# Kernel tuning notes

Hardware: AMD Instinct MI355X
Metric: run time of the kernel (lower is better)

## Reference

```python
import jax, jax.numpy as jnp
import numpy as np

# Performer/FAVOR+ style linear attention constants (from module __init__)
A_CONST = 0.1
S_CONST = 1.0
B_CONST = (S_CONST * (1.0 - 4.0 * A_CONST)) ** 0.5  # sqrt(0.6)
C_CONST = -(S_CONST + 1.0) / 2.0                    # -1.0

R = 256     # number of random features
D = 64      # head / feature dim
L = 65536   # sequence length
DV = 64     # value dim
SCALE = 0.125  # keep ||q||^2 ~ 1 so exp stays well-conditioned


def setup_inputs() -> dict:
    key = jax.random.key(0)
    kq, kk, kv, kw = jax.random.split(key, 4)
    Q = jax.random.normal(kq, (D, L), dtype=jnp.float32) * SCALE
    K = jax.random.normal(kk, (D, L), dtype=jnp.float32) * SCALE
    V = jax.random.normal(kv, (L, DV), dtype=jnp.float32)
    W = jax.random.normal(kw, (R, D), dtype=jnp.float32)  # random feature projections
    return {"Q": Q, "K": K, "V": V, "W": W}


def _phi(W, X, c):
    # X: [d, L]; W: [r, d] -> features [r, L]
    d = X.shape[0]
    D_norm = (1.0 - 4.0 * A_CONST) ** (d / 4.0)  # pow(pow(1-4A,0.25), d)
    sq = jnp.sum(X * X, axis=0)                  # [L], diag of X^T X
    return D_norm * jnp.exp(A_CONST + B_CONST * (W @ X) + c * sq)


def reference(Q, K, V, W):
    phiK = _phi(W, K, C_CONST * S_CONST)  # f2: [r, Lk]
    kv = phiK @ V                          # [r, dv]
    phiQ = _phi(W, Q, C_CONST)             # f1: [r, Lq]
    return phiQ.T @ kv                     # [Lq, dv]
```

## Files before the change

kernel.cpp:

```cpp
#include <hip/hip_runtime.h>

typedef _Float16 f16;
typedef __attribute__((ext_vector_type(8))) _Float16 f16x8;
typedef __attribute__((ext_vector_type(4))) _Float16 f16x4;
typedef __attribute__((ext_vector_type(4))) float f32x4;

#define BARRIER()                                              \
    do {                                                       \
        asm volatile("s_waitcnt lgkmcnt(0)" ::: "memory");     \
        __builtin_amdgcn_s_barrier();                          \
        __builtin_amdgcn_sched_barrier(0);                     \
    } while (0)

namespace {
constexpr int kL   = 65536;
constexpr int kR   = 256;
constexpr int kD   = 64;
constexpr int kDV  = 64;

constexpr int kChunks  = 4;
constexpr int kABlocks = 256;
constexpr int kBBlocks = 256;
constexpr int kRBlocks = 128;

constexpr float kBc   = 0.7745966692414834f;
constexpr float kBase0 = -1.1417405264f;
constexpr float kOutScale = 9.5367431640625e-7f;
}

__global__ __launch_bounds__(512, 2)
void favor_kv(const float* __restrict__ Kg, const float* __restrict__ Vg,
              const float* __restrict__ Wg, f16* __restrict__ partials)
{
    __shared__ f16 sXt[2][64 * 64];
    __shared__ f16 sVt[3][64 * 64];
    __shared__ f16 sPhi[2][256 * 64];
    __shared__ float sRed[2][8 * 64];
    __shared__ float sRedT[2][64];

    const int tid  = threadIdx.x;
    const int w    = tid >> 6;
    const int lane = tid & 63;
    const int l15  = lane & 15;
    const int lhi  = lane >> 4;
    const int blk  = blockIdx.x;
    const int lblk = blk * (64 * kChunks);

    const int scol  = lane;
    const int dbase = w * 8;
    const int wr = w >> 1;
    const int wc = w & 1;

    float ka[2][8], va[2][8];
    auto issueLoads = [&](int c) {
        const int l0 = lblk + c * 64;
        const int p  = c & 1;
#pragma unroll
        for (int j = 0; j < 8; ++j) ka[p][j] = Kg[(dbase + j) * kL + l0 + scol];
#pragma unroll
        for (int j = 0; j < 8; ++j) va[p][j] = Vg[(size_t)(l0 + dbase + j) * kDV + scol];
    };

    issueLoads(0);
    issueLoads(1);

    f16x8 wfrag[2][2];
#pragma unroll
    for (int ri = 0; ri < 2; ++ri)
#pragma unroll
        for (int ks = 0; ks < 2; ++ks) {
            const float* p = Wg + (32 * w + 16 * ri + l15) * kD + 32 * ks + 8 * lhi;
            f16x8 v;
#pragma unroll
            for (int j = 0; j < 8; ++j) v[j] = (f16)p[j];
            wfrag[ri][ks] = v;
        }

    f32x4 acc[4][2];
#pragma unroll
    for (int a = 0; a < 4; ++a)
#pragma unroll
        for (int d = 0; d < 2; ++d) { f32x4 z0 = {0.f, 0.f, 0.f, 0.f}; acc[a][d] = z0; }

    auto stage = [&](int c) {
        const int p  = c & 1;
        const int pv3 = c % 3;
        float s = 0.f;
        f16x8 hk, hv;
#pragma unroll
        for (int j = 0; j < 8; ++j) {
            const float x = ka[p][j];
            s += x * x;
            hk[j] = (f16)x;
            hv[j] = (f16)va[p][j];
        }
        sRed[p][w * 64 + scol] = s;
        *(f16x8*)&sXt[p][scol * 64 + (dbase ^ ((scol & 7) << 3))] = hk;
        *(f16x8*)&sVt[pv3][scol * 64 + (dbase ^ ((scol & 7) << 3))] = hv;
    };

    auto norms = [&](int c) {
        const int p = c & 1;
        float sqv = 0.f;
#pragma unroll
        for (int g = 0; g < 8; ++g) sqv += sRed[p][g * 64 + lane];
        sRedT[p][lane] = sqv;
    };

    auto zphi = [&](int c) {
        const int p = c & 1;
        f16x8 bfr[2][4];
#pragma unroll
        for (int ks = 0; ks < 2; ++ks)
#pragma unroll
            for (int lf = 0; lf < 4; ++lf) {
                const int row = 16 * lf + l15;
                bfr[ks][lf] = *(const f16x8*)&sXt[p][row * 64 + ((32 * ks + 8 * lhi) ^ ((row & 7) << 3))];
            }
#pragma unroll
        for (int ri = 0; ri < 2; ++ri) {
            f32x4 z[4];
#pragma unroll
            for (int lf = 0; lf < 4; ++lf) { f32x4 z0 = {0.f, 0.f, 0.f, 0.f}; z[lf] = z0; }
            __builtin_amdgcn_s_setprio(1);
#pragma unroll
            for (int ks = 0; ks < 2; ++ks)
#pragma unroll
                for (int lf = 0; lf < 4; ++lf)
                    z[lf] = __builtin_amdgcn_mfma_f32_16x16x32_f16(bfr[ks][lf], wfrag[ri][ks], z[lf], 0, 0, 0);
            __builtin_amdgcn_s_setprio(0);
            const int r = 32 * w + 16 * ri + l15;
#pragma unroll
            for (int lf = 0; lf < 4; ++lf) {
                const f32x4 sq4 = *(const f32x4*)&sRedT[p][16 * lf + 4 * lhi];
                f16x4 ph;
#pragma unroll
                for (int j = 0; j < 4; ++j)
                    ph[j] = (f16)__expf(fmaf(z[lf][j], kBc, kBase0 - sq4[j]));
                const int lbase = 16 * lf + 4 * lhi;
                *(f16x4*)&sPhi[p][r * 64 + (lbase ^ ((r & 7) << 3))] = ph;
            }
        }
    };

    auto pv = [&](int c) {
        const int p  = c & 1;
        const int pv3 = c % 3;
        __builtin_amdgcn_s_setprio(1);
#pragma unroll
        for (int ks = 0; ks < 2; ++ks) {
            f16x8 af[4], bf[2];
#pragma unroll
            for (int ai = 0; ai < 4; ++ai) {
                const int r = 64 * wr + 16 * ai + l15;
                af[ai] = *(const f16x8*)&sPhi[p][r * 64 + ((32 * ks + 8 * lhi) ^ ((r & 7) << 3))];
            }
#pragma unroll
            for (int di = 0; di < 2; ++di) {
                const int dv = 32 * wc + 16 * di + l15;
                bf[di] = *(const f16x8*)&sVt[pv3][dv * 64 + ((32 * ks + 8 * lhi) ^ ((dv & 7) << 3))];
            }
#pragma unroll
            for (int ai = 0; ai < 4; ++ai)
#pragma unroll
                for (int di = 0; di < 2; ++di)
                    acc[ai][di] = __builtin_amdgcn_mfma_f32_16x16x32_f16(af[ai], bf[di], acc[ai][di], 0, 0, 0);
        }
        __builtin_amdgcn_s_setprio(0);
    };

    stage(0);
    BARRIER();
#pragma unroll
    for (int c = 0; c < kChunks; ++c) {
        if (c > 0) pv(c - 1);
        norms(c);
        zphi(c);
        if (c + 1 < kChunks) stage(c + 1);
        if (c + 2 < kChunks) issueLoads(c + 2);
        BARRIER();
    }
    pv(kChunks - 1);

    f16* po = partials + (size_t)blk * (kR * kDV);
#pragma unroll
    for (int ai = 0; ai < 4; ++ai)
#pragma unroll
        for (int di = 0; di < 2; ++di) {
            const int dv = 32 * wc + 16 * di + l15;
            f16x4 pk;
#pragma unroll
            for (int j = 0; j < 4; ++j) pk[j] = (f16)acc[ai][di][j];
            *(f16x4*)&po[dv * kR + 64 * wr + 16 * ai + 4 * lhi] = pk;
        }
}

__global__ __launch_bounds__(512)
void favor_reduce(const f16* __restrict__ partials, f16* __restrict__ kvT,
                  const float* __restrict__ Wg, f16* __restrict__ Wp)
{
    __shared__ float sAcc[32][128];
    const int tid  = threadIdx.x;
    const int slot = tid & 15;
    const int g    = tid >> 4;

    if (blockIdx.x == 0) {
#pragma unroll
        for (int it = 0; it < 4; ++it) {
            const int idx    = tid + it * 512;
            const int fragid = idx >> 6;
            const int ln     = idx & 63;
            const int rf = fragid >> 1, ks = fragid & 1;
            const float* src = Wg + (16 * rf + (ln & 15)) * kD + 32 * ks + 8 * (ln >> 4);
            f16x8 v;
#pragma unroll
            for (int j = 0; j < 8; ++j) v[j] = (f16)src[j];
            *(f16x8*)&Wp[(size_t)idx * 8] = v;
        }
    }

    const size_t obase = (size_t)blockIdx.x * 128 + slot * 8;
    float a[8] = {0.f, 0.f, 0.f, 0.f, 0.f, 0.f, 0.f, 0.f};
#pragma unroll 4
    for (int i = 0; i < 8; ++i) {
        const int s = g * 8 + i;
        const f16x8 v = *(const f16x8*)&partials[(size_t)s * (kR * kDV) + obase];
#pragma unroll
        for (int j = 0; j < 8; ++j) a[j] += (float)v[j];
    }
#pragma unroll
    for (int j = 0; j < 8; ++j) sAcc[g][slot * 8 + j] = a[j];
    __syncthreads();

    if (tid < 128) {
        float tot = 0.f;
#pragma unroll
        for (int gg = 0; gg < 32; ++gg) tot += sAcc[gg][tid];
        kvT[(size_t)blockIdx.x * 128 + tid] = (f16)tot;
    }
}

__global__ __launch_bounds__(512, 2)
void favor_out(const float* __restrict__ Qg, const f16* __restrict__ Wp,
               const f16* __restrict__ kvT, float* __restrict__ outg)
{
    __shared__ f16 sXt[2][64 * 64];
    __shared__ f16 sPhiT[2][64 * 256];
    __shared__ float sRed[2][8 * 64];

    const int tid  = threadIdx.x;
    const int w    = tid >> 6;
    const int lane = tid & 63;
    const int l15  = lane & 15;
    const int lhi  = lane >> 4;
    const int blk  = blockIdx.x;
    const int lblk = blk * (64 * kChunks);

    const int scol  = lane;
    const int dbase = w * 8;
    const int lfo = w >> 1;
    const int dvh = w & 1;

    float qa[2][8];
    auto issueLoads = [&](int c) {
        const int l0 = lblk + c * 64;
        const int p  = c & 1;
#pragma unroll
        for (int j = 0; j < 8; ++j) qa[p][j] = Qg[(dbase + j) * kL + l0 + scol];
    };

    issueLoads(0);
    issueLoads(1);

    f16x8 kvf[2][8];
#pragma unroll
    for (int di = 0; di < 2; ++di) {
        const int dv = 32 * dvh + 16 * di + l15;
#pragma unroll
        for (int ks = 0; ks < 8; ++ks)
            kvf[di][ks] = *(const f16x8*)&kvT[dv * kR + 32 * ks + 8 * lhi];
    }

    f16x8 wfrag[2][2];
#pragma unroll
    for (int ri = 0; ri < 2; ++ri)
#pragma unroll
        for (int ks = 0; ks < 2; ++ks)
            wfrag[ri][ks] = *(const f16x8*)&Wp[(size_t)((((2 * w + ri) * 2 + ks) * 64) + lane) * 8];

    auto stageQ = [&](int c) {
        const int p = c & 1;
        float s = 0.f;
        f16x8 hq;
#pragma unroll
        for (int j = 0; j < 8; ++j) {
            const float x = qa[p][j];
            s += x * x;
            hq[j] = (f16)x;
        }
        sRed[p][w * 64 + scol] = s;
        *(f16x8*)&sXt[p][scol * 64 + (dbase ^ ((scol & 7) << 3))] = hq;
    };

    auto zphiQ = [&](int c) {
        const int p = c & 1;
        float sqv = 0.f;
#pragma unroll
        for (int g = 0; g < 8; ++g) sqv += sRed[p][g * 64 + lane];
        float tbase[4];
#pragma unroll
        for (int lf = 0; lf < 4; ++lf)
            tbase[lf] = kBase0 - __shfl(sqv, lf * 16 + l15, 64);

        f16x8 bfr[2][4];
#pragma unroll
        for (int ks = 0; ks < 2; ++ks)
#pragma unroll
            for (int lf = 0; lf < 4; ++lf) {
                const int row = 16 * lf + l15;
                bfr[ks][lf] = *(const f16x8*)&sXt[p][row * 64 + ((32 * ks + 8 * lhi) ^ ((row & 7) << 3))];
            }
#pragma unroll
        for (int ri = 0; ri < 2; ++ri) {
            f32x4 z[4];
#pragma unroll
            for (int lf = 0; lf < 4; ++lf) { f32x4 z0 = {0.f, 0.f, 0.f, 0.f}; z[lf] = z0; }
            __builtin_amdgcn_s_setprio(1);
#pragma unroll
            for (int ks = 0; ks < 2; ++ks)
#pragma unroll
                for (int lf = 0; lf < 4; ++lf)
                    z[lf] = __builtin_amdgcn_mfma_f32_16x16x32_f16(wfrag[ri][ks], bfr[ks][lf], z[lf], 0, 0, 0);
            __builtin_amdgcn_s_setprio(0);
            const int r0 = 32 * w + 16 * ri + 4 * lhi;
#pragma unroll
            for (int lf = 0; lf < 4; ++lf) {
                const int lc = 16 * lf + l15;
                f16x4 ph;
#pragma unroll
                for (int j = 0; j < 4; ++j)
                    ph[j] = (f16)__expf(fmaf(z[lf][j], kBc, tbase[lf]));
                *(f16x4*)&sPhiT[p][lc * 256 + (r0 ^ ((lc & 7) << 3))] = ph;
            }
        }
    };

    auto pvOut = [&](int c) {
        const int p = c & 1;
        f32x4 oA[2], oB[2];
        { f32x4 z0 = {0.f, 0.f, 0.f, 0.f}; oA[0] = z0; oA[1] = z0; oB[0] = z0; oB[1] = z0; }
        const int lrow = 16 * lfo + l15;
        __builtin_amdgcn_s_setprio(1);
#pragma unroll
        for (int ks = 0; ks < 4; ++ks) {
            const f16x8 afA = *(const f16x8*)&sPhiT[p][lrow * 256 + ((32 * ks + 8 * lhi) ^ ((lrow & 7) << 3))];
            const f16x8 afB = *(const f16x8*)&sPhiT[p][lrow * 256 + ((32 * (ks + 4) + 8 * lhi) ^ ((lrow & 7) << 3))];
#pragma unroll
            for (int di = 0; di < 2; ++di) {
                oA[di] = __builtin_amdgcn_mfma_f32_16x16x32_f16(afA, kvf[di][ks], oA[di], 0, 0, 0);
                oB[di] = __builtin_amdgcn_mfma_f32_16x16x32_f16(afB, kvf[di][ks + 4], oB[di], 0, 0, 0);
            }
        }
        __builtin_amdgcn_s_setprio(0);
        const int l0 = lblk + c * 64;
#pragma unroll
        for (int di = 0; di < 2; ++di) {
            const f32x4 o2 = oA[di] + oB[di];
#pragma unroll
            for (int j = 0; j < 4; ++j) {
                const int ll = 16 * lfo + 4 * lhi + j;
                const int dv = 32 * dvh + 16 * di + l15;
                outg[(size_t)(l0 + ll) * kDV + dv] = o2[j] * kOutScale;
            }
        }
    };

    stageQ(0);
    BARRIER();
#pragma unroll
    for (int c = 0; c < kChunks; ++c) {
        if (c > 0) pvOut(c - 1);
        zphiQ(c);
        if (c + 1 < kChunks) stageQ(c + 1);
        if (c + 2 < kChunks) issueLoads(c + 2);
        BARRIER();
    }
    pvOut(kChunks - 1);
}

extern "C" void kernel_launch(void* const* d_in, const int* in_sizes, int n_in,
                              void* d_out, int out_size, void* d_ws, size_t ws_size,
                              hipStream_t stream)
{
    const float* Q = (const float*)d_in[0];
    const float* K = (const float*)d_in[1];
    const float* V = (const float*)d_in[2];
    const float* W = (const float*)d_in[3];
    float* out = (float*)d_out;

    f16* partials = (f16*)d_ws;
    f16* kvT = (f16*)((char*)d_ws + (size_t)kABlocks * kR * kDV * sizeof(f16));
    f16* Wp  = kvT + (size_t)kR * kDV;

    favor_kv<<<kABlocks, 512, 0, stream>>>(K, V, W, partials);
    favor_reduce<<<kRBlocks, 512, 0, stream>>>(partials, kvT, W, Wp);
    favor_out<<<kBBlocks, 512, 0, stream>>>(Q, Wp, kvT, out);

    (void)in_sizes; (void)n_in; (void)out_size; (void)ws_size;
}
```

Measured before the change: 35.92 us.

## Load Q directly into MFMA B-fragments, dropping LDS staging and reduction

After: 36.56 us. No clear change (+1.8%).

```diff
diff --git a/kernel.cpp b/kernel.cpp
--- a/kernel.cpp
+++ b/kernel.cpp
@@ -244,9 +244,7 @@
 void favor_out(const float* __restrict__ Qg, const f16* __restrict__ Wp,
                const f16* __restrict__ kvT, float* __restrict__ outg)
 {
-    __shared__ f16 sXt[2][64 * 64];
     __shared__ f16 sPhiT[2][64 * 256];
-    __shared__ float sRed[2][8 * 64];
 
     const int tid  = threadIdx.x;
     const int w    = tid >> 6;
@@ -256,21 +254,43 @@
     const int blk  = blockIdx.x;
     const int lblk = blk * (64 * kChunks);
 
-    const int scol  = lane;
-    const int dbase = w * 8;
+    const int lfq   = w & 3;
+    const int rhalf = w >> 2;
     const int lfo = w >> 1;
     const int dvh = w & 1;
 
-    float qa[2][8];
-    auto issueLoads = [&](int c) {
-        const int l0 = lblk + c * 64;
-        const int p  = c & 1;
-#pragma unroll
-        for (int j = 0; j < 8; ++j) qa[p][j] = Qg[(dbase + j) * kL + l0 + scol];
-    };
-
-    issueLoads(0);
-    issueLoads(1);
+    float vq[16];
+    auto issueQ = [&](int c) {
+        const int l0 = lblk + c * 64 + 16 * lfq + l15;
+#pragma unroll
+        for (int ks = 0; ks < 2; ++ks)
+#pragma unroll
+            for (int j = 0; j < 8; ++j)
+                vq[ks * 8 + j] = Qg[(32 * ks + 8 * lhi + j) * kL + l0];
+    };
+
+    f16x8 qfrag[2][2];
+    float tb[2];
+    auto cvtQ = [&](int c) {
+        const int p = c & 1;
+        float s = 0.f;
+#pragma unroll
+        for (int ks = 0; ks < 2; ++ks) {
+            f16x8 h;
+#pragma unroll
+            for (int j = 0; j < 8; ++j) {
+                const float x = vq[ks * 8 + j];
+                s += x * x;
+                h[j] = (f16)x;
+            }
+            qfrag[p][ks] = h;
+        }
+        s += __shfl_xor(s, 16);
+        s += __shfl_xor(s, 32);
+        tb[p] = kBase0 - s;
+    };
+
+    issueQ(0);
 
     f16x8 kvf[2][8];
 #pragma unroll
@@ -281,68 +301,35 @@
             kvf[di][ks] = *(const f16x8*)&kvT[dv * kR + 32 * ks + 8 * lhi];
     }
 
-    f16x8 wfrag[2][2];
-#pragma unroll
-    for (int ri = 0; ri < 2; ++ri)
-#pragma unroll
-        for (int ks = 0; ks < 2; ++ks)
-            wfrag[ri][ks] = *(const f16x8*)&Wp[(size_t)((((2 * w + ri) * 2 + ks) * 64) + lane) * 8];
-
-    auto stageQ = [&](int c) {
-        const int p = c & 1;
-        float s = 0.f;
-        f16x8 hq;
-#pragma unroll
-        for (int j = 0; j < 8; ++j) {
-            const float x = qa[p][j];
-            s += x * x;
-            hq[j] = (f16)x;
-        }
-        sRed[p][w * 64 + scol] = s;
-        *(f16x8*)&sXt[p][scol * 64 + (dbase ^ ((scol & 7) << 3))] = hq;
-    };
+    f16x8 wfrag[8][2];
+#pragma unroll
+    for (int f = 0; f < 8; ++f)
+#pragma unroll
+        for (int ks = 0; ks < 2; ++ks) {
+            const int rf = rhalf * 8 + f;
+            wfrag[f][ks] = *(const f16x8*)&Wp[(size_t)(((rf * 2 + ks) * 64) + lane) * 8];
+        }
+
+    cvtQ(0);
 
     auto zphiQ = [&](int c) {
         const int p = c & 1;
-        float sqv = 0.f;
-#pragma unroll
-        for (int g = 0; g < 8; ++g) sqv += sRed[p][g * 64 + lane];
-        float tbase[4];
-#pragma unroll
-        for (int lf = 0; lf < 4; ++lf)
-            tbase[lf] = kBase0 - __shfl(sqv, lf * 16 + l15, 64);
-
-        f16x8 bfr[2][4];
-#pragma unroll
-        for (int ks = 0; ks < 2; ++ks)
-#pragma unroll
-            for (int lf = 0; lf < 4; ++lf) {
-                const int row = 16 * lf + l15;
-                bfr[ks][lf] = *(const f16x8*)&sXt[p][row * 64 + ((32 * ks + 8 * lhi) ^ ((row & 7) << 3))];
-            }
-#pragma unroll
-        for (int ri = 0; ri < 2; ++ri) {
-            f32x4 z[4];
-#pragma unroll
-            for (int lf = 0; lf < 4; ++lf) { f32x4 z0 = {0.f, 0.f, 0.f, 0.f}; z[lf] = z0; }
-            __builtin_amdgcn_s_setprio(1);
-#pragma unroll
-            for (int ks = 0; ks < 2; ++ks)
-#pragma unroll
-                for (int lf = 0; lf < 4; ++lf)
-                    z[lf] = __builtin_amdgcn_mfma_f32_16x16x32_f16(wfrag[ri][ks], bfr[ks][lf], z[lf], 0, 0, 0);
-            __builtin_amdgcn_s_setprio(0);
-            const int r0 = 32 * w + 16 * ri + 4 * lhi;
-#pragma unroll
-            for (int lf = 0; lf < 4; ++lf) {
-                const int lc = 16 * lf + l15;
-                f16x4 ph;
-#pragma unroll
-                for (int j = 0; j < 4; ++j)
-                    ph[j] = (f16)__expf(fmaf(z[lf][j], kBc, tbase[lf]));
-                *(f16x4*)&sPhiT[p][lc * 256 + (r0 ^ ((lc & 7) << 3))] = ph;
-            }
-        }
+        const int lc = 16 * lfq + l15;
+        const int m  = (lc & 7) << 3;
+        __builtin_amdgcn_s_setprio(1);
+#pragma unroll
+        for (int f = 0; f < 8; ++f) {
+            f32x4 z = {0.f, 0.f, 0.f, 0.f};
+            z = __builtin_amdgcn_mfma_f32_16x16x32_f16(wfrag[f][0], qfrag[p][0], z, 0, 0, 0);
+            z = __builtin_amdgcn_mfma_f32_16x16x32_f16(wfrag[f][1], qfrag[p][1], z, 0, 0, 0);
+            const int r0 = rhalf * 128 + f * 16 + 4 * lhi;
+            f16x4 ph;
+#pragma unroll
+            for (int j = 0; j < 4; ++j)
+                ph[j] = (f16)__expf(fmaf(z[j], kBc, tb[p]));
+            *(f16x4*)&sPhiT[p][lc * 256 + (r0 ^ m)] = ph;
+        }
+        __builtin_amdgcn_s_setprio(0);
     };
 
     auto pvOut = [&](int c) {
@@ -350,11 +337,12 @@
         f32x4 oA[2], oB[2];
         { f32x4 z0 = {0.f, 0.f, 0.f, 0.f}; oA[0] = z0; oA[1] = z0; oB[0] = z0; oB[1] = z0; }
         const int lrow = 16 * lfo + l15;
+        const int m = (lrow & 7) << 3;
         __builtin_amdgcn_s_setprio(1);
 #pragma unroll
         for (int ks = 0; ks < 4; ++ks) {
-            const f16x8 afA = *(const f16x8*)&sPhiT[p][lrow * 256 + ((32 * ks + 8 * lhi) ^ ((lrow & 7) << 3))];
-            const f16x8 afB = *(const f16x8*)&sPhiT[p][lrow * 256 + ((32 * (ks + 4) + 8 * lhi) ^ ((lrow & 7) << 3))];
+            const f16x8 afA = *(const f16x8*)&sPhiT[p][lrow * 256 + ((32 * ks + 8 * lhi) ^ m)];
+            const f16x8 afB = *(const f16x8*)&sPhiT[p][lrow * 256 + ((32 * (ks + 4) + 8 * lhi) ^ m)];
 #pragma unroll
             for (int di = 0; di < 2; ++di) {
                 oA[di] = __builtin_amdgcn_mfma_f32_16x16x32_f16(afA, kvf[di][ks], oA[di], 0, 0, 0);
@@ -375,15 +363,13 @@
         }
     };
 
-    stageQ(0);
-    BARRIER();
 #pragma unroll
     for (int c = 0; c < kChunks; ++c) {
         if (c > 0) pvOut(c - 1);
         zphiQ(c);
-        if (c + 1 < kChunks) stageQ(c + 1);
-        if (c + 2 < kChunks) issueLoads(c + 2);
+        if (c + 1 < kChunks) issueQ(c + 1);
         BARRIER();
+        if (c + 1 < kChunks) cvtQ(c + 1);
     }
     pvOut(kChunks - 1);
 }
```

## Replace partials buffer and reduce kernel with float atomics into kv accumulator

Applied to the files above, without the earlier changes.

New measurement: 137.1 us. 282% more time.

```diff
diff --git a/kernel.cpp b/kernel.cpp
--- a/kernel.cpp
+++ b/kernel.cpp
@@ -21,7 +21,6 @@
 constexpr int kChunks  = 4;
 constexpr int kABlocks = 256;
 constexpr int kBBlocks = 256;
-constexpr int kRBlocks = 128;
 
 constexpr float kBc   = 0.7745966692414834f;
 constexpr float kBase0 = -1.1417405264f;
@@ -30,7 +29,8 @@
 
 __global__ __launch_bounds__(512, 2)
 void favor_kv(const float* __restrict__ Kg, const float* __restrict__ Vg,
-              const float* __restrict__ Wg, f16* __restrict__ partials)
+              const float* __restrict__ Wg, float* __restrict__ kvAcc,
+              f16* __restrict__ Wp)
 {
     __shared__ f16 sXt[2][64 * 64];
     __shared__ f16 sVt[3][64 * 64];
@@ -50,6 +50,21 @@
     const int dbase = w * 8;
     const int wr = w >> 1;
     const int wc = w & 1;
+
+    if (blk == 0) {
+#pragma unroll
+        for (int it = 0; it < 4; ++it) {
+            const int idx    = tid + it * 512;
+            const int fragid = idx >> 6;
+            const int ln     = idx & 63;
+            const int rf = fragid >> 1, ks = fragid & 1;
+            const float* src = Wg + (16 * rf + (ln & 15)) * kD + 32 * ks + 8 * (ln >> 4);
+            f16x8 v;
+#pragma unroll
+            for (int j = 0; j < 8; ++j) v[j] = (f16)src[j];
+            *(f16x8*)&Wp[(size_t)idx * 8] = v;
+        }
+    }
 
     float ka[2][8], va[2][8];
     auto issueLoads = [&](int c) {
@@ -182,67 +197,21 @@
     }
     pv(kChunks - 1);
 
-    f16* po = partials + (size_t)blk * (kR * kDV);
 #pragma unroll
     for (int ai = 0; ai < 4; ++ai)
 #pragma unroll
         for (int di = 0; di < 2; ++di) {
             const int dv = 32 * wc + 16 * di + l15;
-            f16x4 pk;
-#pragma unroll
-            for (int j = 0; j < 4; ++j) pk[j] = (f16)acc[ai][di][j];
-            *(f16x4*)&po[dv * kR + 64 * wr + 16 * ai + 4 * lhi] = pk;
-        }
-}
-
-__global__ __launch_bounds__(512)
-void favor_reduce(const f16* __restrict__ partials, f16* __restrict__ kvT,
-                  const float* __restrict__ Wg, f16* __restrict__ Wp)
-{
-    __shared__ float sAcc[32][128];
-    const int tid  = threadIdx.x;
-    const int slot = tid & 15;
-    const int g    = tid >> 4;
-
-    if (blockIdx.x == 0) {
-#pragma unroll
-        for (int it = 0; it < 4; ++it) {
-            const int idx    = tid + it * 512;
-            const int fragid = idx >> 6;
-            const int ln     = idx & 63;
-            const int rf = fragid >> 1, ks = fragid & 1;
-            const float* src = Wg + (16 * rf + (ln & 15)) * kD + 32 * ks + 8 * (ln >> 4);
-            f16x8 v;
-#pragma unroll
-            for (int j = 0; j < 8; ++j) v[j] = (f16)src[j];
-            *(f16x8*)&Wp[(size_t)idx * 8] = v;
-        }
-    }
-
-    const size_t obase = (size_t)blockIdx.x * 128 + slot * 8;
-    float a[8] = {0.f, 0.f, 0.f, 0.f, 0.f, 0.f, 0.f, 0.f};
-#pragma unroll 4
-    for (int i = 0; i < 8; ++i) {
-        const int s = g * 8 + i;
-        const f16x8 v = *(const f16x8*)&partials[(size_t)s * (kR * kDV) + obase];
-#pragma unroll
-        for (int j = 0; j < 8; ++j) a[j] += (float)v[j];
-    }
-#pragma unroll
-    for (int j = 0; j < 8; ++j) sAcc[g][slot * 8 + j] = a[j];
-    __syncthreads();
-
-    if (tid < 128) {
-        float tot = 0.f;
-#pragma unroll
-        for (int gg = 0; gg < 32; ++gg) tot += sAcc[gg][tid];
-        kvT[(size_t)blockIdx.x * 128 + tid] = (f16)tot;
-    }
+            const int rb = 64 * wr + 16 * ai + 4 * lhi;
+#pragma unroll
+            for (int j = 0; j < 4; ++j)
+                atomicAdd(&kvAcc[dv * kR + rb + j], acc[ai][di][j]);
+        }
 }
 
 __global__ __launch_bounds__(512, 2)
 void favor_out(const float* __restrict__ Qg, const f16* __restrict__ Wp,
-               const f16* __restrict__ kvT, float* __restrict__ outg)
+               const float* __restrict__ kvAcc, float* __restrict__ outg)
 {
     __shared__ f16 sXt[2][64 * 64];
     __shared__ f16 sPhiT[2][64 * 256];
@@ -277,8 +246,13 @@
     for (int di = 0; di < 2; ++di) {
         const int dv = 32 * dvh + 16 * di + l15;
 #pragma unroll
-        for (int ks = 0; ks < 8; ++ks)
-            kvf[di][ks] = *(const f16x8*)&kvT[dv * kR + 32 * ks + 8 * lhi];
+        for (int ks = 0; ks < 8; ++ks) {
+            const float* src = kvAcc + dv * kR + 32 * ks + 8 * lhi;
+            f16x8 h;
+#pragma unroll
+            for (int j = 0; j < 8; ++j) h[j] = (f16)src[j];
+            kvf[di][ks] = h;
+        }
     }
 
     f16x8 wfrag[2][2];
@@ -398,13 +372,12 @@
     const float* W = (const float*)d_in[3];
     float* out = (float*)d_out;
 
-    f16* partials = (f16*)d_ws;
-    f16* kvT = (f16*)((char*)d_ws + (size_t)kABlocks * kR * kDV * sizeof(f16));
-    f16* Wp  = kvT + (size_t)kR * kDV;
-
-    favor_kv<<<kABlocks, 512, 0, stream>>>(K, V, W, partials);
-    favor_reduce<<<kRBlocks, 512, 0, stream>>>(partials, kvT, W, Wp);
-    favor_out<<<kBBlocks, 512, 0, stream>>>(Q, Wp, kvT, out);
+    float* kvAcc = (float*)d_ws;
+    f16* Wp = (f16*)((char*)d_ws + (size_t)kR * kDV * sizeof(float));
+
+    hipMemsetAsync(kvAcc, 0, (size_t)kR * kDV * sizeof(float), stream);
+    favor_kv<<<kABlocks, 512, 0, stream>>>(K, V, W, kvAcc, Wp);
+    favor_out<<<kBBlocks, 512, 0, stream>>>(Q, Wp, kvAcc, out);
 
     (void)in_sizes; (void)n_in; (void)out_size; (void)ws_size;
 }
```
